# Kernel tuning notes

Hardware: AMD Instinct MI355X
Metric: run time of the kernel (lower is better)

Reference implementation:

```python
import jax, jax.numpy as jnp
import numpy as np

N = 100000   # nodes
E = 1600000  # edges
F_IN = 128
H = 128      # hidden_channels
G = 1000     # graphs in batch
EPS = 1e-5


def setup_inputs() -> dict:
    key = jax.random.key(0)
    ks = jax.random.split(key, 20)
    x = jax.random.normal(ks[0], (N, F_IN), dtype=jnp.float32)
    edge_index = jax.random.randint(ks[1], (2, E), 0, N, dtype=jnp.int64)
    batch = jnp.sort(jax.random.randint(ks[2], (N,), 0, G, dtype=jnp.int64))
    s = 0.05
    inp = {
        "x": x,
        "edge_index": edge_index,
        "batch": batch,
        "W1": jax.random.normal(ks[3], (F_IN, H), dtype=jnp.float32) * s,
        "b1": jnp.zeros((H,), jnp.float32),
        "g1": jnp.ones((H,), jnp.float32),
        "be1": jnp.zeros((H,), jnp.float32),
        "W2": jax.random.normal(ks[4], (H, H), dtype=jnp.float32) * s,
        "b2": jnp.zeros((H,), jnp.float32),
        "g2": jnp.ones((H,), jnp.float32),
        "be2": jnp.zeros((H,), jnp.float32),
        "W3": jax.random.normal(ks[5], (H, H), dtype=jnp.float32) * s,
        "b3": jnp.zeros((H,), jnp.float32),
        "g3": jnp.ones((H,), jnp.float32),
        "be3": jnp.zeros((H,), jnp.float32),
        "Wl": jax.random.normal(ks[6], (H, 1), dtype=jnp.float32) * s,
        "bl": jnp.zeros((1,), jnp.float32),
    }
    return inp


def _gcn_conv(x, W, b, src, dst, dinv):
    # PyG GCNConv: h = x W; out[d] = sum_e dinv[src]*dinv[dst]*h[src]; out += b
    h = x @ W
    coef = (dinv[src] * dinv[dst])[:, None]
    msg = h[src] * coef                       # [E+N, H] gather + scale
    out = jax.ops.segment_sum(msg, dst, num_segments=N)
    return out + b


def _bn_relu(x, g, be):
    # BatchNorm1d training mode: batch stats, biased variance
    m = jnp.mean(x, axis=0)
    v = jnp.var(x, axis=0)
    xn = (x - m) * jax.lax.rsqrt(v + EPS)
    return jax.nn.relu(xn * g + be)


def reference(x, edge_index, batch, W1, b1, g1, be1, W2, b2, g2, be2,
              W3, b3, g3, be3, Wl, bl):
    loop = jnp.arange(N, dtype=edge_index.dtype)
    src = jnp.concatenate([edge_index[0], loop])  # self-loops appended
    dst = jnp.concatenate([edge_index[1], loop])
    deg = jax.ops.segment_sum(jnp.ones_like(dst, dtype=x.dtype), dst,
                              num_segments=N)
    dinv = jax.lax.rsqrt(deg)                     # deg >= 1 (self-loops)

    h = _bn_relu(_gcn_conv(x, W1, b1, src, dst, dinv), g1, be1)
    h = _bn_relu(_gcn_conv(h, W2, b2, src, dst, dinv), g2, be2)
    h = _bn_relu(_gcn_conv(h, W3, b3, src, dst, dinv), g3, be3)

    # global_mean_pool over graph ids
    sums = jax.ops.segment_sum(h, batch, num_segments=G)
    cnt = jax.ops.segment_sum(jnp.ones((N,), h.dtype), batch, num_segments=G)
    pooled = sums / jnp.maximum(cnt, 1.0)[:, None]

    return pooled @ Wl + bl
```

## Files before the change

kernel.cpp:

```cpp
#include <hip/hip_runtime.h>
#include <hip/hip_bf16.h>

#define Nn 100000
#define Ee 1600000
#define Hh 128
#define Gg 1000
#define EPSb 1e-5f

#define SCAN_CHUNK 1024
#define NB_SCAN 98
#define AGG_BLOCKS 2048
#define GEMM_BLOCKS 782

typedef unsigned int uint;
typedef short short8 __attribute__((ext_vector_type(8)));
typedef float floatx4 __attribute__((ext_vector_type(4)));

static __device__ __forceinline__ uint bf16rne(float f) {
    uint u = __float_as_uint(f);
    return (u + 0x7fffu + ((u >> 16) & 1u)) >> 16;
}
static __device__ __forceinline__ float bflo(uint u) { return __uint_as_float(u << 16); }
static __device__ __forceinline__ float bfhi(uint u) { return __uint_as_float(u & 0xffff0000u); }


__global__ void k_init(int* __restrict__ deg, int* __restrict__ cursor,
                       float* __restrict__ colsum) {
    int i = blockIdx.x * blockDim.x + threadIdx.x;
    if (i < Nn) { deg[i] = 1; cursor[i] = 0; }
    if (i < 768) colsum[i] = 0.f;
}

__global__ void k_deg(const int* __restrict__ dst, int* __restrict__ deg) {
    int i = blockIdx.x * blockDim.x + threadIdx.x;
    if (i < Ee) atomicAdd(&deg[dst[i]], 1);
}

__global__ void k_scan1(const int* __restrict__ deg, int* __restrict__ bsum) {
    __shared__ int ls[256];
    int t = threadIdx.x;
    int base = blockIdx.x * SCAN_CHUNK + t * 4;
    int s = 0;
#pragma unroll
    for (int j = 0; j < 4; ++j) { int i = base + j; if (i < Nn) s += deg[i]; }
    ls[t] = s;
    __syncthreads();
    for (int off = 128; off; off >>= 1) {
        if (t < off) ls[t] += ls[t + off];
        __syncthreads();
    }
    if (t == 0) bsum[blockIdx.x] = ls[0];
}

__global__ void k_scan2(int* __restrict__ bsum) {
    __shared__ int ls[128];
    int t = threadIdx.x;
    int v = (t < NB_SCAN) ? bsum[t] : 0;
    ls[t] = v;
    __syncthreads();
    for (int off = 1; off < 128; off <<= 1) {
        int u = (t >= off) ? ls[t - off] : 0;
        __syncthreads();
        ls[t] += u;
        __syncthreads();
    }
    if (t < NB_SCAN) bsum[t] = ls[t] - v;
}

__global__ void k_scan3(const int* __restrict__ deg, const int* __restrict__ bsum,
                        int* __restrict__ offs, float* __restrict__ dinv) {
    __shared__ int ls[256];
    int t = threadIdx.x;
    int base = blockIdx.x * SCAN_CHUNK + t * 4;
    int d[4]; int s = 0;
#pragma unroll
    for (int j = 0; j < 4; ++j) {
        int i = base + j;
        d[j] = (i < Nn) ? deg[i] : 0;
        s += d[j];
    }
    ls[t] = s;
    __syncthreads();
    for (int off = 1; off < 256; off <<= 1) {
        int u = (t >= off) ? ls[t - off] : 0;
        __syncthreads();
        ls[t] += u;
        __syncthreads();
    }
    int run = bsum[blockIdx.x] + ls[t] - s;
#pragma unroll
    for (int j = 0; j < 4; ++j) {
        int i = base + j;
        if (i < Nn) {
            offs[i] = run;
            dinv[i] = rsqrtf((float)d[j]);
        }
        run += d[j];
    }
    if (blockIdx.x == 0 && t == 0) offs[Nn] = Ee + Nn;
}

__global__ void k_fill(const int* __restrict__ src, const int* __restrict__ dst,
                       const int* __restrict__ offs, int* __restrict__ cursor,
                       const float* __restrict__ dinv,
                       int2* __restrict__ adj) {
    int i = blockIdx.x * blockDim.x + threadIdx.x;
    if (i >= Ee + Nn) return;
    int s, d;
    if (i < Ee) { s = src[i]; d = dst[i]; }
    else        { s = d = i - Ee; }
    int pos = offs[d] + atomicAdd(&cursor[d], 1);
    adj[pos] = make_int2(s, __float_as_int(dinv[s] * dinv[d]));
}


__global__ void k_wconv3(const float* __restrict__ W1, const float* __restrict__ W2,
                         const float* __restrict__ W3, uint* __restrict__ Wt) {
    int idx = blockIdx.x * blockDim.x + threadIdx.x;
    if (idx >= 3 * 8192) return;
    const float* W = (idx < 8192) ? W1 : ((idx < 16384) ? W2 : W3);
    int k = idx & 8191;
    int n = k >> 6, ku = k & 63;
    uint lo = bf16rne(W[(size_t)(2 * ku) * 128 + n]);
    uint hi = bf16rne(W[(size_t)(2 * ku + 1) * 128 + n]);
    Wt[(size_t)(idx >> 13) * 8192 + n * 64 + ku] = lo | (hi << 16);
}


__global__ __launch_bounds__(256) void k_gemm(
    const float* __restrict__ inf, const uint* __restrict__ inb,
    const uint* __restrict__ Wtp,
    const float* __restrict__ cs, const float* __restrict__ gg,
    const float* __restrict__ be,
    uint* __restrict__ outb, int mode) {
    __shared__ uint XT[128][64];
    __shared__ uint WT[128][64];
    __shared__ float scsh[256];
    int t = threadIdx.x;
    int rowBase = blockIdx.x * 128;
    int r = t >> 1, half = t & 1;

    if (mode) {
        if (t < 128) {
            float s = cs[t], q = cs[128 + t];
            float m = s * (1.0f / Nn);
            float var = q * (1.0f / Nn) - m * m;
            float istd = rsqrtf(var + EPSb);
            float sc = istd * gg[t];
            scsh[t] = sc;
            scsh[128 + t] = fmaf(-m, sc, be[t]);
        }
        __syncthreads();
    }

    {
        int gr = rowBase + r;
        int grc = gr < Nn ? gr : Nn - 1;
        if (mode == 0) {
            const float* sp = inf + (size_t)grc * 128 + half * 64;
#pragma unroll
            for (int q = 0; q < 8; ++q) {
                float4 v0 = *(const float4*)(sp + q * 8);
                float4 v1 = *(const float4*)(sp + q * 8 + 4);
                uint4 o;
                o.x = bf16rne(v0.x) | (bf16rne(v0.y) << 16);
                o.y = bf16rne(v0.z) | (bf16rne(v0.w) << 16);
                o.z = bf16rne(v1.x) | (bf16rne(v1.y) << 16);
                o.w = bf16rne(v1.z) | (bf16rne(v1.w) << 16);
                int g = half * 8 + q;
                *(uint4*)&XT[r][(g ^ (r & 7)) << 2] = o;
            }
        } else {
            const uint* sp = inb + (size_t)grc * 64 + half * 32;
#pragma unroll
            for (int q = 0; q < 8; ++q) {
                uint4 v = *(const uint4*)(sp + q * 4);
                int fb = half * 64 + q * 8;
                float av[8] = {bflo(v.x), bfhi(v.x), bflo(v.y), bfhi(v.y),
                               bflo(v.z), bfhi(v.z), bflo(v.w), bfhi(v.w)};
                uint o[4];
#pragma unroll
                for (int k2 = 0; k2 < 4; ++k2) {
                    float lo = fmaxf(fmaf(av[2 * k2], scsh[fb + 2 * k2],
                                          scsh[128 + fb + 2 * k2]), 0.f);
                    float hi = fmaxf(fmaf(av[2 * k2 + 1], scsh[fb + 2 * k2 + 1],
                                          scsh[128 + fb + 2 * k2 + 1]), 0.f);
                    o[k2] = bf16rne(lo) | (bf16rne(hi) << 16);
                }
                uint4 ov = make_uint4(o[0], o[1], o[2], o[3]);
                int g = half * 8 + q;
                *(uint4*)&XT[r][(g ^ (r & 7)) << 2] = ov;
            }
        }
    }
    {
        const uint* sp = Wtp + (size_t)r * 64 + half * 32;
#pragma unroll
        for (int q = 0; q < 8; ++q) {
            uint4 v = *(const uint4*)(sp + q * 4);
            int g = half * 8 + q;
            *(uint4*)&WT[r][(g ^ (r & 7)) << 2] = v;
        }
    }
    __syncthreads();

    int l = t & 63, w = t >> 6;
    int nb = (w >> 1) * 64;
    int fb2 = (w & 1) * 64;
    int lr = l & 15, lk = l >> 4;
    floatx4 zero = {0.f, 0.f, 0.f, 0.f};
    floatx4 acc[4][4];
#pragma unroll
    for (int mi = 0; mi < 4; ++mi)
#pragma unroll
        for (int ni = 0; ni < 4; ++ni) acc[mi][ni] = zero;

#pragma unroll
    for (int kc = 0; kc < 4; ++kc) {
        short8 xf[4], wf[4];
        int g = kc * 4 + lk;
#pragma unroll
        for (int mi = 0; mi < 4; ++mi) {
            int rr = nb + mi * 16 + lr;
            xf[mi] = *(const short8*)&XT[rr][(g ^ (rr & 7)) << 2];
        }
#pragma unroll
        for (int ni = 0; ni < 4; ++ni) {
            int rr = fb2 + ni * 16 + lr;
            wf[ni] = *(const short8*)&WT[rr][(g ^ (rr & 7)) << 2];
        }
#pragma unroll
        for (int mi = 0; mi < 4; ++mi)
#pragma unroll
            for (int ni = 0; ni < 4; ++ni)
                acc[mi][ni] = __builtin_amdgcn_mfma_f32_16x16x32_bf16(
                    wf[ni], xf[mi], acc[mi][ni], 0, 0, 0);
    }

#pragma unroll
    for (int mi = 0; mi < 4; ++mi) {
        int node = rowBase + nb + mi * 16 + lr;
        if (node < Nn) {
            uint* op = outb + (size_t)node * 64;
#pragma unroll
            for (int ni = 0; ni < 4; ++ni) {
                int fo = fb2 + ni * 16 + lk * 4;
                uint2 o;
                o.x = bf16rne(acc[mi][ni][0]) | (bf16rne(acc[mi][ni][1]) << 16);
                o.y = bf16rne(acc[mi][ni][2]) | (bf16rne(acc[mi][ni][3]) << 16);
                *(uint2*)(op + (fo >> 1)) = o;
            }
        }
    }
}


__global__ __launch_bounds__(256) void k_agg(
    const uint* __restrict__ h32, const int* __restrict__ offs,
    const int2* __restrict__ adj,
    const float* __restrict__ bias, uint* __restrict__ agg,
    float* __restrict__ colsum) {
    __shared__ float ls[256];
    int tid = threadIdx.x;
    ls[tid] = 0.f;
    __syncthreads();
    int lane = tid & 63;
    int gw = blockIdx.x * 4 + (tid >> 6);
    int nw = AGG_BLOCKS * 4;
    int c0 = lane * 2;
    float b0 = bias[c0], b1 = bias[c0 + 1];
    float ps0 = 0.f, pq0 = 0.f, ps1 = 0.f, pq1 = 0.f;
    for (int d = gw; d < Nn; d += nw) {
        int beg = offs[d], end = offs[d + 1];
        float a0 = 0.f, a1 = 0.f;
        int i = beg;
        for (; i + 8 <= end; i += 8) {
            int2 e[8];
#pragma unroll
            for (int j = 0; j < 8; ++j) e[j] = adj[i + j];
            uint hv[8];
#pragma unroll
            for (int j = 0; j < 8; ++j)
                hv[j] = h32[(size_t)e[j].x * 64 + lane];
#pragma unroll
            for (int j = 0; j < 8; ++j) {
                float w = __int_as_float(e[j].y);
                a0 = fmaf(w, bflo(hv[j]), a0);
                a1 = fmaf(w, bfhi(hv[j]), a1);
            }
        }
        for (; i < end; ++i) {
            int2 e = adj[i];
            uint hv = h32[(size_t)e.x * 64 + lane];
            float w = __int_as_float(e.y);
            a0 = fmaf(w, bflo(hv), a0);
            a1 = fmaf(w, bfhi(hv), a1);
        }
        a0 += b0; a1 += b1;
        agg[(size_t)d * 64 + lane] = bf16rne(a0) | (bf16rne(a1) << 16);
        ps0 += a0; pq0 += a0 * a0;
        ps1 += a1; pq1 += a1 * a1;
    }
    atomicAdd(&ls[c0], ps0);
    atomicAdd(&ls[c0 + 1], ps1);
    atomicAdd(&ls[128 + c0], pq0);
    atomicAdd(&ls[128 + c0 + 1], pq1);
    __syncthreads();
    atomicAdd(&colsum[tid], ls[tid]);
}


__global__ __launch_bounds__(256) void k_pool(
    const uint* __restrict__ agg, const int* __restrict__ batch,
    const float* __restrict__ cs, const float* __restrict__ gg,
    const float* __restrict__ be,
    const float* __restrict__ Wl, const float* __restrict__ bl,
    float* __restrict__ out) {
    __shared__ float scsh[256];
    int tid = threadIdx.x;
    if (tid < 128) {
        float s = cs[tid], q = cs[128 + tid];
        float m = s * (1.0f / Nn);
        float var = q * (1.0f / Nn) - m * m;
        float istd = rsqrtf(var + EPSb);
        float sc = istd * gg[tid];
        scsh[tid] = sc;
        scsh[128 + tid] = fmaf(-m, sc, be[tid]);
    }
    __syncthreads();
    int lane = tid & 63;
    int g = (blockIdx.x * blockDim.x + tid) >> 6;
    if (g >= Gg) return;
    int lo = 0, hi = Nn;
    while (lo < hi) { int mid = (lo + hi) >> 1; if (batch[mid] < g) lo = mid + 1; else hi = mid; }
    int beg = lo;
    hi = Nn;
    while (lo < hi) { int mid = (lo + hi) >> 1; if (batch[mid] < g + 1) lo = mid + 1; else hi = mid; }
    int end = lo;
    int c0 = lane * 2;
    float sc0 = scsh[c0], sh0 = scsh[128 + c0];
    float sc1 = scsh[c0 + 1], sh1 = scsh[128 + c0 + 1];
    float s0 = 0.f, s1 = 0.f;
    for (int n = beg; n < end; ++n) {
        uint v = agg[(size_t)n * 64 + lane];
        s0 += fmaxf(fmaf(bflo(v), sc0, sh0), 0.f);
        s1 += fmaxf(fmaf(bfhi(v), sc1, sh1), 0.f);
    }
    float inv = 1.0f / fmaxf((float)(end - beg), 1.0f);
    float part = (s0 * inv) * Wl[c0] + (s1 * inv) * Wl[c0 + 1];
#pragma unroll
    for (int off = 32; off; off >>= 1) part += __shfl_down(part, off);
    if (lane == 0) out[g] = part + bl[0];
}


extern "C" void kernel_launch(void* const* d_in, const int* in_sizes, int n_in,
                              void* d_out, int out_size, void* d_ws, size_t ws_size,
                              hipStream_t stream) {
    const float* x   = (const float*)d_in[0];
    const int*   ei  = (const int*)d_in[1];
    const int*   src = ei;
    const int*   dst = ei + Ee;
    const int*   bat = (const int*)d_in[2];
    const float* W1 = (const float*)d_in[3];
    const float* b1 = (const float*)d_in[4];
    const float* g1 = (const float*)d_in[5];
    const float* be1 = (const float*)d_in[6];
    const float* W2 = (const float*)d_in[7];
    const float* b2 = (const float*)d_in[8];
    const float* g2 = (const float*)d_in[9];
    const float* be2 = (const float*)d_in[10];
    const float* W3 = (const float*)d_in[11];
    const float* b3 = (const float*)d_in[12];
    const float* g3 = (const float*)d_in[13];
    const float* be3 = (const float*)d_in[14];
    const float* Wl = (const float*)d_in[15];
    const float* bl = (const float*)d_in[16];
    float* out = (float*)d_out;

    char* w = (char*)d_ws;
    auto alloc = [&](size_t bytes) {
        void* p = (void*)w;
        w += (bytes + 255) & ~(size_t)255;
        return p;
    };
    int*   deg    = (int*)alloc((size_t)Nn * 4);
    int*   cursor = (int*)alloc((size_t)Nn * 4);
    int*   offs   = (int*)alloc((size_t)(Nn + 1) * 4);
    int*   bsum   = (int*)alloc(256 * 4);
    float* dinv   = (float*)alloc((size_t)Nn * 4);
    float* colsum = (float*)alloc(768 * 4);
    uint*  Wt     = (uint*)alloc((size_t)3 * 8192 * 4);
    int2*  adj    = (int2*)alloc((size_t)(Ee + Nn) * 8);
    uint*  tmp    = (uint*)alloc((size_t)Nn * 64 * 4);
    uint*  agg    = (uint*)alloc((size_t)Nn * 64 * 4);

    float* csA = colsum;
    float* csB = colsum + 256;
    float* csC = colsum + 512;

    k_init<<<(Nn + 255) / 256, 256, 0, stream>>>(deg, cursor, colsum);
    k_deg<<<(Ee + 255) / 256, 256, 0, stream>>>(dst, deg);
    k_scan1<<<NB_SCAN, 256, 0, stream>>>(deg, bsum);
    k_scan2<<<1, 128, 0, stream>>>(bsum);
    k_scan3<<<NB_SCAN, 256, 0, stream>>>(deg, bsum, offs, dinv);
    k_fill<<<(Ee + Nn + 255) / 256, 256, 0, stream>>>(src, dst, offs, cursor, dinv, adj);
    k_wconv3<<<96, 256, 0, stream>>>(W1, W2, W3, Wt);
    k_gemm<<<GEMM_BLOCKS, 256, 0, stream>>>(x, (const uint*)0, Wt,
                                            (const float*)0, (const float*)0,
                                            (const float*)0, tmp, 0);
    k_agg<<<AGG_BLOCKS, 256, 0, stream>>>(tmp, offs, adj, b1, agg, csA);
    k_gemm<<<GEMM_BLOCKS, 256, 0, stream>>>((const float*)0, agg, Wt + 8192,
                                            csA, g1, be1, tmp, 1);
    k_agg<<<AGG_BLOCKS, 256, 0, stream>>>(tmp, offs, adj, b2, agg, csB);
    k_gemm<<<GEMM_BLOCKS, 256, 0, stream>>>((const float*)0, agg, Wt + 16384,
                                            csB, g2, be2, tmp, 1);
    k_agg<<<AGG_BLOCKS, 256, 0, stream>>>(tmp, offs, adj, b3, agg, csC);
    k_pool<<<(Gg * 64 + 255) / 256, 256, 0, stream>>>(agg, bat, csC, g3, be3,
                                                      Wl, bl, out);
}
```

Before: 598.5 us.

## Gather 16-byte row slices across four edge groups per wave in aggregation

Each wave now splits into four 16-lane groups that each take a different edge. Every lane loads a uint4 (8 bf16 features) per edge instead of one uint, and the groups' partial sums are combined with cross-lane shuffles before lane group 0 writes the row and updates the BN statistics. The aim is wider, fewer gather instructions and more edges in flight per wave in the memory-bound aggregation. The cost is extra shuffle reductions and predicated tail handling that does masked loads. Only a quarter of the lanes do the final store and stats work.

```diff
diff --git a/kernel.cpp b/kernel.cpp
--- a/kernel.cpp
+++ b/kernel.cpp
@@ -10,9 +10,11 @@
 #define SCAN_CHUNK 1024
 #define NB_SCAN 98
 #define AGG_BLOCKS 2048
+#define NWAVES (AGG_BLOCKS * 4)
 #define GEMM_BLOCKS 782
 
 typedef unsigned int uint;
+typedef unsigned long long u64;
 typedef short short8 __attribute__((ext_vector_type(8)));
 typedef float floatx4 __attribute__((ext_vector_type(4)));
 
@@ -265,46 +267,93 @@
     ls[tid] = 0.f;
     __syncthreads();
     int lane = tid & 63;
-    int gw = blockIdx.x * 4 + (tid >> 6);
-    int nw = AGG_BLOCKS * 4;
-    int c0 = lane * 2;
-    float b0 = bias[c0], b1 = bias[c0 + 1];
-    float ps0 = 0.f, pq0 = 0.f, ps1 = 0.f, pq1 = 0.f;
-    for (int d = gw; d < Nn; d += nw) {
+    int g = lane >> 4;
+    int c = lane & 15;
+    int wv = blockIdx.x * 4 + (tid >> 6);
+    const uint4* h4 = (const uint4*)h32;
+    const u64* adj8 = (const u64*)adj;
+    int f0 = c * 8;
+    float bb[8];
+#pragma unroll
+    for (int j = 0; j < 8; ++j) bb[j] = bias[f0 + j];
+    float ps[8], pq[8];
+#pragma unroll
+    for (int j = 0; j < 8; ++j) { ps[j] = 0.f; pq[j] = 0.f; }
+
+    for (int d = wv; d < Nn; d += NWAVES) {
         int beg = offs[d], end = offs[d + 1];
-        float a0 = 0.f, a1 = 0.f;
+        float acc[8];
+#pragma unroll
+        for (int j = 0; j < 8; ++j) acc[j] = 0.f;
         int i = beg;
         for (; i + 8 <= end; i += 8) {
-            int2 e[8];
-#pragma unroll
-            for (int j = 0; j < 8; ++j) e[j] = adj[i + j];
-            uint hv[8];
-#pragma unroll
-            for (int j = 0; j < 8; ++j)
-                hv[j] = h32[(size_t)e[j].x * 64 + lane];
+            u64 eA = adj8[i + g];
+            u64 eB = adj8[i + 4 + g];
+            uint4 hA = h4[(size_t)(uint)eA * 16 + c];
+            uint4 hB = h4[(size_t)(uint)eB * 16 + c];
+            float wA = __uint_as_float((uint)(eA >> 32));
+            float wB = __uint_as_float((uint)(eB >> 32));
+            acc[0] = fmaf(wA, bflo(hA.x), acc[0]);
+            acc[1] = fmaf(wA, bfhi(hA.x), acc[1]);
+            acc[2] = fmaf(wA, bflo(hA.y), acc[2]);
+            acc[3] = fmaf(wA, bfhi(hA.y), acc[3]);
+            acc[4] = fmaf(wA, bflo(hA.z), acc[4]);
+            acc[5] = fmaf(wA, bfhi(hA.z), acc[5]);
+            acc[6] = fmaf(wA, bflo(hA.w), acc[6]);
+            acc[7] = fmaf(wA, bfhi(hA.w), acc[7]);
+            acc[0] = fmaf(wB, bflo(hB.x), acc[0]);
+            acc[1] = fmaf(wB, bfhi(hB.x), acc[1]);
+            acc[2] = fmaf(wB, bflo(hB.y), acc[2]);
+            acc[3] = fmaf(wB, bfhi(hB.y), acc[3]);
+            acc[4] = fmaf(wB, bflo(hB.z), acc[4]);
+            acc[5] = fmaf(wB, bfhi(hB.z), acc[5]);
+            acc[6] = fmaf(wB, bflo(hB.w), acc[6]);
+            acc[7] = fmaf(wB, bfhi(hB.w), acc[7]);
+        }
+        for (; i < end; i += 4) {
+            int idx = i + g;
+            int ok = idx < end;
+            u64 e = adj8[ok ? idx : (end - 1)];
+            uint4 hv = h4[(size_t)(uint)e * 16 + c];
+            float w = ok ? __uint_as_float((uint)(e >> 32)) : 0.f;
+            acc[0] = fmaf(w, bflo(hv.x), acc[0]);
+            acc[1] = fmaf(w, bfhi(hv.x), acc[1]);
+            acc[2] = fmaf(w, bflo(hv.y), acc[2]);
+            acc[3] = fmaf(w, bfhi(hv.y), acc[3]);
+            acc[4] = fmaf(w, bflo(hv.z), acc[4]);
+            acc[5] = fmaf(w, bfhi(hv.z), acc[5]);
+            acc[6] = fmaf(w, bflo(hv.w), acc[6]);
+            acc[7] = fmaf(w, bfhi(hv.w), acc[7]);
+        }
+#pragma unroll
+        for (int j = 0; j < 8; ++j) {
+            acc[j] += __shfl_xor(acc[j], 16);
+            acc[j] += __shfl_xor(acc[j], 32);
+        }
+        if (g == 0) {
+            float a[8];
+#pragma unroll
+            for (int j = 0; j < 8; ++j) a[j] = acc[j] + bb[j];
+            uint4 o;
+            o.x = bf16rne(a[0]) | (bf16rne(a[1]) << 16);
+            o.y = bf16rne(a[2]) | (bf16rne(a[3]) << 16);
+            o.z = bf16rne(a[4]) | (bf16rne(a[5]) << 16);
+            o.w = bf16rne(a[6]) | (bf16rne(a[7]) << 16);
+            *(uint4*)(agg + (size_t)d * 64 + c * 4) = o;
 #pragma unroll
             for (int j = 0; j < 8; ++j) {
-                float w = __int_as_float(e[j].y);
-                a0 = fmaf(w, bflo(hv[j]), a0);
-                a1 = fmaf(w, bfhi(hv[j]), a1);
+                ps[j] += a[j];
+                pq[j] += a[j] * a[j];
             }
         }
-        for (; i < end; ++i) {
-            int2 e = adj[i];
-            uint hv = h32[(size_t)e.x * 64 + lane];
-            float w = __int_as_float(e.y);
-            a0 = fmaf(w, bflo(hv), a0);
-            a1 = fmaf(w, bfhi(hv), a1);
-        }
-        a0 += b0; a1 += b1;
-        agg[(size_t)d * 64 + lane] = bf16rne(a0) | (bf16rne(a1) << 16);
-        ps0 += a0; pq0 += a0 * a0;
-        ps1 += a1; pq1 += a1 * a1;
-    }
-    atomicAdd(&ls[c0], ps0);
-    atomicAdd(&ls[c0 + 1], ps1);
-    atomicAdd(&ls[128 + c0], pq0);
-    atomicAdd(&ls[128 + c0 + 1], pq1);
+    }
+    if (g == 0) {
+#pragma unroll
+        for (int j = 0; j < 8; ++j) {
+            atomicAdd(&ls[f0 + j], ps[j]);
+            atomicAdd(&ls[128 + f0 + j], pq[j]);
+        }
+    }
     __syncthreads();
     atomicAdd(&colsum[tid], ls[tid]);
 }
```

After: 647.5 us. 1.08x slower.

## Process two row tiles per GEMM block with prefetch; merge scan passes and memset init

Applied to the files above, without the earlier changes.

The GEMM kernel now handles two 128-row tiles per block, with half as many blocks. It loads the second tile's inputs into registers while the first tile's MFMAs run, so the global-load latency is hidden and the weight tile is loaded once for both. The init kernel is replaced by a single hipMemsetAsync over deg, cursor and colsum, and the self-loop +1 is folded into the scan reads. The separate block-sum scan kernel is merged into scan3, which saves launches. In exchange, registers rise from holding the prefetched tile (launch bounds set to 2 blocks per SM), and every scan3 block redundantly rescans the block sums.

```diff
diff --git a/kernel.cpp b/kernel.cpp
--- a/kernel.cpp
+++ b/kernel.cpp
@@ -10,7 +10,8 @@
 #define SCAN_CHUNK 1024
 #define NB_SCAN 98
 #define AGG_BLOCKS 2048
-#define GEMM_BLOCKS 782
+#define NWAVES (AGG_BLOCKS * 4)
+#define GEMM_BLOCKS 391
 
 typedef unsigned int uint;
 typedef short short8 __attribute__((ext_vector_type(8)));
@@ -23,13 +24,6 @@
 static __device__ __forceinline__ float bflo(uint u) { return __uint_as_float(u << 16); }
 static __device__ __forceinline__ float bfhi(uint u) { return __uint_as_float(u & 0xffff0000u); }
 
-
-__global__ void k_init(int* __restrict__ deg, int* __restrict__ cursor,
-                       float* __restrict__ colsum) {
-    int i = blockIdx.x * blockDim.x + threadIdx.x;
-    if (i < Nn) { deg[i] = 1; cursor[i] = 0; }
-    if (i < 768) colsum[i] = 0.f;
-}
 
 __global__ void k_deg(const int* __restrict__ dst, int* __restrict__ deg) {
     int i = blockIdx.x * blockDim.x + threadIdx.x;
@@ -42,7 +36,7 @@
     int base = blockIdx.x * SCAN_CHUNK + t * 4;
     int s = 0;
 #pragma unroll
-    for (int j = 0; j < 4; ++j) { int i = base + j; if (i < Nn) s += deg[i]; }
+    for (int j = 0; j < 4; ++j) { int i = base + j; if (i < Nn) s += deg[i] + 1; }
     ls[t] = s;
     __syncthreads();
     for (int off = 128; off; off >>= 1) {
@@ -52,42 +46,36 @@
     if (t == 0) bsum[blockIdx.x] = ls[0];
 }
 
-__global__ void k_scan2(int* __restrict__ bsum) {
-    __shared__ int ls[128];
-    int t = threadIdx.x;
-    int v = (t < NB_SCAN) ? bsum[t] : 0;
-    ls[t] = v;
-    __syncthreads();
-    for (int off = 1; off < 128; off <<= 1) {
-        int u = (t >= off) ? ls[t - off] : 0;
-        __syncthreads();
-        ls[t] += u;
-        __syncthreads();
-    }
-    if (t < NB_SCAN) bsum[t] = ls[t] - v;
-}
-
 __global__ void k_scan3(const int* __restrict__ deg, const int* __restrict__ bsum,
                         int* __restrict__ offs, float* __restrict__ dinv) {
     __shared__ int ls[256];
+    __shared__ int bs[128];
     int t = threadIdx.x;
+    if (t < 128) bs[t] = (t < NB_SCAN) ? bsum[t] : 0;
     int base = blockIdx.x * SCAN_CHUNK + t * 4;
     int d[4]; int s = 0;
 #pragma unroll
     for (int j = 0; j < 4; ++j) {
         int i = base + j;
-        d[j] = (i < Nn) ? deg[i] : 0;
+        d[j] = (i < Nn) ? deg[i] + 1 : 0;
         s += d[j];
     }
     ls[t] = s;
     __syncthreads();
+    for (int off = 1; off < 128; off <<= 1) {
+        int u = (t >= off && t < 128) ? bs[t - off] : 0;
+        __syncthreads();
+        if (t < 128) bs[t] += u;
+        __syncthreads();
+    }
     for (int off = 1; off < 256; off <<= 1) {
         int u = (t >= off) ? ls[t - off] : 0;
         __syncthreads();
         ls[t] += u;
         __syncthreads();
     }
-    int run = bsum[blockIdx.x] + ls[t] - s;
+    int blockBase = (blockIdx.x == 0) ? 0 : bs[blockIdx.x - 1];
+    int run = blockBase + ls[t] - s;
 #pragma unroll
     for (int j = 0; j < 4; ++j) {
         int i = base + j;
@@ -127,7 +115,7 @@
 }
 
 
-__global__ __launch_bounds__(256) void k_gemm(
+__global__ __launch_bounds__(256, 2) void k_gemm(
     const float* __restrict__ inf, const uint* __restrict__ inb,
     const uint* __restrict__ Wtp,
     const float* __restrict__ cs, const float* __restrict__ gg,
@@ -137,61 +125,16 @@
     __shared__ uint WT[128][64];
     __shared__ float scsh[256];
     int t = threadIdx.x;
-    int rowBase = blockIdx.x * 128;
     int r = t >> 1, half = t & 1;
 
-    if (mode) {
-        if (t < 128) {
-            float s = cs[t], q = cs[128 + t];
-            float m = s * (1.0f / Nn);
-            float var = q * (1.0f / Nn) - m * m;
-            float istd = rsqrtf(var + EPSb);
-            float sc = istd * gg[t];
-            scsh[t] = sc;
-            scsh[128 + t] = fmaf(-m, sc, be[t]);
-        }
-        __syncthreads();
-    }
-
-    {
-        int gr = rowBase + r;
-        int grc = gr < Nn ? gr : Nn - 1;
-        if (mode == 0) {
-            const float* sp = inf + (size_t)grc * 128 + half * 64;
-#pragma unroll
-            for (int q = 0; q < 8; ++q) {
-                float4 v0 = *(const float4*)(sp + q * 8);
-                float4 v1 = *(const float4*)(sp + q * 8 + 4);
-                uint4 o;
-                o.x = bf16rne(v0.x) | (bf16rne(v0.y) << 16);
-                o.y = bf16rne(v0.z) | (bf16rne(v0.w) << 16);
-                o.z = bf16rne(v1.x) | (bf16rne(v1.y) << 16);
-                o.w = bf16rne(v1.z) | (bf16rne(v1.w) << 16);
-                int g = half * 8 + q;
-                *(uint4*)&XT[r][(g ^ (r & 7)) << 2] = o;
-            }
-        } else {
-            const uint* sp = inb + (size_t)grc * 64 + half * 32;
-#pragma unroll
-            for (int q = 0; q < 8; ++q) {
-                uint4 v = *(const uint4*)(sp + q * 4);
-                int fb = half * 64 + q * 8;
-                float av[8] = {bflo(v.x), bfhi(v.x), bflo(v.y), bfhi(v.y),
-                               bflo(v.z), bfhi(v.z), bflo(v.w), bfhi(v.w)};
-                uint o[4];
-#pragma unroll
-                for (int k2 = 0; k2 < 4; ++k2) {
-                    float lo = fmaxf(fmaf(av[2 * k2], scsh[fb + 2 * k2],
-                                          scsh[128 + fb + 2 * k2]), 0.f);
-                    float hi = fmaxf(fmaf(av[2 * k2 + 1], scsh[fb + 2 * k2 + 1],
-                                          scsh[128 + fb + 2 * k2 + 1]), 0.f);
-                    o[k2] = bf16rne(lo) | (bf16rne(hi) << 16);
-                }
-                uint4 ov = make_uint4(o[0], o[1], o[2], o[3]);
-                int g = half * 8 + q;
-                *(uint4*)&XT[r][(g ^ (r & 7)) << 2] = ov;
-            }
-        }
+    if (mode && t < 128) {
+        float s = cs[t], q = cs[128 + t];
+        float m = s * (1.0f / Nn);
+        float var = q * (1.0f / Nn) - m * m;
+        float istd = rsqrtf(var + EPSb);
+        float sc = istd * gg[t];
+        scsh[t] = sc;
+        scsh[128 + t] = fmaf(-m, sc, be[t]);
     }
     {
         const uint* sp = Wtp + (size_t)r * 64 + half * 32;
@@ -201,6 +144,57 @@
             int g = half * 8 + q;
             *(uint4*)&WT[r][(g ^ (r & 7)) << 2] = v;
         }
+    }
+
+    float4 xf[16];
+    uint4  xb[8];
+
+    int rb0 = blockIdx.x * 128;
+    {
+        int grc = rb0 + r;
+        if (grc >= Nn) grc = Nn - 1;
+        if (mode == 0) {
+            const float* sp = inf + (size_t)grc * 128 + half * 64;
+#pragma unroll
+            for (int q = 0; q < 8; ++q) {
+                xf[2 * q]     = *(const float4*)(sp + q * 8);
+                xf[2 * q + 1] = *(const float4*)(sp + q * 8 + 4);
+            }
+        } else {
+            const uint* sp = inb + (size_t)grc * 64 + half * 32;
+#pragma unroll
+            for (int q = 0; q < 8; ++q) xb[q] = *(const uint4*)(sp + q * 4);
+        }
+    }
+    __syncthreads();
+
+#pragma unroll
+    for (int q = 0; q < 8; ++q) {
+        uint4 o;
+        if (mode == 0) {
+            float4 v0 = xf[2 * q], v1 = xf[2 * q + 1];
+            o.x = bf16rne(v0.x) | (bf16rne(v0.y) << 16);
+            o.y = bf16rne(v0.z) | (bf16rne(v0.w) << 16);
+            o.z = bf16rne(v1.x) | (bf16rne(v1.y) << 16);
+            o.w = bf16rne(v1.z) | (bf16rne(v1.w) << 16);
+        } else {
+            uint4 v = xb[q];
+            int fb = half * 64 + q * 8;
+            float av[8] = {bflo(v.x), bfhi(v.x), bflo(v.y), bfhi(v.y),
+                           bflo(v.z), bfhi(v.z), bflo(v.w), bfhi(v.w)};
+            uint oo[4];
+#pragma unroll
+            for (int k2 = 0; k2 < 4; ++k2) {
+                float lo = fmaxf(fmaf(av[2 * k2], scsh[fb + 2 * k2],
+                                      scsh[128 + fb + 2 * k2]), 0.f);
+                float hi = fmaxf(fmaf(av[2 * k2 + 1], scsh[fb + 2 * k2 + 1],
+                                      scsh[128 + fb + 2 * k2 + 1]), 0.f);
+                oo[k2] = bf16rne(lo) | (bf16rne(hi) << 16);
+            }
+            o = make_uint4(oo[0], oo[1], oo[2], oo[3]);
+        }
+        int g = half * 8 + q;
+        *(uint4*)&XT[r][(g ^ (r & 7)) << 2] = o;
     }
     __syncthreads();
 
@@ -209,46 +203,140 @@
     int fb2 = (w & 1) * 64;
     int lr = l & 15, lk = l >> 4;
     floatx4 zero = {0.f, 0.f, 0.f, 0.f};
-    floatx4 acc[4][4];
-#pragma unroll
-    for (int mi = 0; mi < 4; ++mi)
-#pragma unroll
-        for (int ni = 0; ni < 4; ++ni) acc[mi][ni] = zero;
-
-#pragma unroll
-    for (int kc = 0; kc < 4; ++kc) {
-        short8 xf[4], wf[4];
-        int g = kc * 4 + lk;
+
+    int rb1 = (blockIdx.x + GEMM_BLOCKS) * 128;
+    {
+        int grc = rb1 + r;
+        if (grc >= Nn) grc = Nn - 1;
+        if (mode == 0) {
+            const float* sp = inf + (size_t)grc * 128 + half * 64;
+#pragma unroll
+            for (int q = 0; q < 8; ++q) {
+                xf[2 * q]     = *(const float4*)(sp + q * 8);
+                xf[2 * q + 1] = *(const float4*)(sp + q * 8 + 4);
+            }
+        } else {
+            const uint* sp = inb + (size_t)grc * 64 + half * 32;
+#pragma unroll
+            for (int q = 0; q < 8; ++q) xb[q] = *(const uint4*)(sp + q * 4);
+        }
+    }
+
+    {
+        floatx4 acc[4][4];
+#pragma unroll
+        for (int mi = 0; mi < 4; ++mi)
+#pragma unroll
+            for (int ni = 0; ni < 4; ++ni) acc[mi][ni] = zero;
+#pragma unroll
+        for (int kc = 0; kc < 4; ++kc) {
+            short8 xfr[4], wfr[4];
+            int g = kc * 4 + lk;
+#pragma unroll
+            for (int mi = 0; mi < 4; ++mi) {
+                int rr = nb + mi * 16 + lr;
+                xfr[mi] = *(const short8*)&XT[rr][(g ^ (rr & 7)) << 2];
+            }
+#pragma unroll
+            for (int ni = 0; ni < 4; ++ni) {
+                int rr = fb2 + ni * 16 + lr;
+                wfr[ni] = *(const short8*)&WT[rr][(g ^ (rr & 7)) << 2];
+            }
+#pragma unroll
+            for (int mi = 0; mi < 4; ++mi)
+#pragma unroll
+                for (int ni = 0; ni < 4; ++ni)
+                    acc[mi][ni] = __builtin_amdgcn_mfma_f32_16x16x32_bf16(
+                        wfr[ni], xfr[mi], acc[mi][ni], 0, 0, 0);
+        }
 #pragma unroll
         for (int mi = 0; mi < 4; ++mi) {
-            int rr = nb + mi * 16 + lr;
-            xf[mi] = *(const short8*)&XT[rr][(g ^ (rr & 7)) << 2];
-        }
-#pragma unroll
-        for (int ni = 0; ni < 4; ++ni) {
-            int rr = fb2 + ni * 16 + lr;
-            wf[ni] = *(const short8*)&WT[rr][(g ^ (rr & 7)) << 2];
-        }
+            int node = rb0 + nb + mi * 16 + lr;
+            if (node < Nn) {
+                uint* op = outb + (size_t)node * 64;
+#pragma unroll
+                for (int ni = 0; ni < 4; ++ni) {
+                    int fo = fb2 + ni * 16 + lk * 4;
+                    uint2 o;
+                    o.x = bf16rne(acc[mi][ni][0]) | (bf16rne(acc[mi][ni][1]) << 16);
+                    o.y = bf16rne(acc[mi][ni][2]) | (bf16rne(acc[mi][ni][3]) << 16);
+                    *(uint2*)(op + (fo >> 1)) = o;
+                }
+            }
+        }
+    }
+    __syncthreads();
+
+#pragma unroll
+    for (int q = 0; q < 8; ++q) {
+        uint4 o;
+        if (mode == 0) {
+            float4 v0 = xf[2 * q], v1 = xf[2 * q + 1];
+            o.x = bf16rne(v0.x) | (bf16rne(v0.y) << 16);
+            o.y = bf16rne(v0.z) | (bf16rne(v0.w) << 16);
+            o.z = bf16rne(v1.x) | (bf16rne(v1.y) << 16);
+            o.w = bf16rne(v1.z) | (bf16rne(v1.w) << 16);
+        } else {
+            uint4 v = xb[q];
+            int fb = half * 64 + q * 8;
+            float av[8] = {bflo(v.x), bfhi(v.x), bflo(v.y), bfhi(v.y),
+                           bflo(v.z), bfhi(v.z), bflo(v.w), bfhi(v.w)};
+            uint oo[4];
+#pragma unroll
+            for (int k2 = 0; k2 < 4; ++k2) {
+                float lo = fmaxf(fmaf(av[2 * k2], scsh[fb + 2 * k2],
+                                      scsh[128 + fb + 2 * k2]), 0.f);
+                float hi = fmaxf(fmaf(av[2 * k2 + 1], scsh[fb + 2 * k2 + 1],
+                                      scsh[128 + fb + 2 * k2 + 1]), 0.f);
+                oo[k2] = bf16rne(lo) | (bf16rne(hi) << 16);
+            }
+            o = make_uint4(oo[0], oo[1], oo[2], oo[3]);
+        }
+        int g = half * 8 + q;
+        *(uint4*)&XT[r][(g ^ (r & 7)) << 2] = o;
+    }
+    __syncthreads();
+
+    {
+        floatx4 acc[4][4];
 #pragma unroll
         for (int mi = 0; mi < 4; ++mi)
 #pragma unroll
-            for (int ni = 0; ni < 4; ++ni)
-                acc[mi][ni] = __builtin_amdgcn_mfma_f32_16x16x32_bf16(
-                    wf[ni], xf[mi], acc[mi][ni], 0, 0, 0);
-    }
-
-#pragma unroll
-    for (int mi = 0; mi < 4; ++mi) {
-        int node = rowBase + nb + mi * 16 + lr;
-        if (node < Nn) {
-            uint* op = outb + (size_t)node * 64;
+            for (int ni = 0; ni < 4; ++ni) acc[mi][ni] = zero;
+#pragma unroll
+        for (int kc = 0; kc < 4; ++kc) {
+            short8 xfr[4], wfr[4];
+            int g = kc * 4 + lk;
+#pragma unroll
+            for (int mi = 0; mi < 4; ++mi) {
+                int rr = nb + mi * 16 + lr;
+                xfr[mi] = *(const short8*)&XT[rr][(g ^ (rr & 7)) << 2];
+            }
 #pragma unroll
             for (int ni = 0; ni < 4; ++ni) {
-                int fo = fb2 + ni * 16 + lk * 4;
-                uint2 o;
-                o.x = bf16rne(acc[mi][ni][0]) | (bf16rne(acc[mi][ni][1]) << 16);
-                o.y = bf16rne(acc[mi][ni][2]) | (bf16rne(acc[mi][ni][3]) << 16);
-                *(uint2*)(op + (fo >> 1)) = o;
+                int rr = fb2 + ni * 16 + lr;
+                wfr[ni] = *(const short8*)&WT[rr][(g ^ (rr & 7)) << 2];
+            }
+#pragma unroll
+            for (int mi = 0; mi < 4; ++mi)
+#pragma unroll
+                for (int ni = 0; ni < 4; ++ni)
+                    acc[mi][ni] = __builtin_amdgcn_mfma_f32_16x16x32_bf16(
+                        wfr[ni], xfr[mi], acc[mi][ni], 0, 0, 0);
+        }
+#pragma unroll
+        for (int mi = 0; mi < 4; ++mi) {
+            int node = rb1 + nb + mi * 16 + lr;
+            if (node < Nn) {
+                uint* op = outb + (size_t)node * 64;
+#pragma unroll
+                for (int ni = 0; ni < 4; ++ni) {
+                    int fo = fb2 + ni * 16 + lk * 4;
+                    uint2 o;
+                    o.x = bf16rne(acc[mi][ni][0]) | (bf16rne(acc[mi][ni][1]) << 16);
+                    o.y = bf16rne(acc[mi][ni][2]) | (bf16rne(acc[mi][ni][3]) << 16);
+                    *(uint2*)(op + (fo >> 1)) = o;
+                }
             }
         }
     }
@@ -266,7 +354,7 @@
     __syncthreads();
     int lane = tid & 63;
     int gw = blockIdx.x * 4 + (tid >> 6);
-    int nw = AGG_BLOCKS * 4;
+    int nw = NWAVES;
     int c0 = lane * 2;
     float b0 = bias[c0], b1 = bias[c0 + 1];
     float ps0 = 0.f, pq0 = 0.f, ps1 = 0.f, pq1 = 0.f;
@@ -386,10 +474,11 @@
     };
     int*   deg    = (int*)alloc((size_t)Nn * 4);
     int*   cursor = (int*)alloc((size_t)Nn * 4);
+    float* colsum = (float*)alloc(768 * 4);
+    size_t zspan  = (size_t)((char*)(colsum + 768) - (char*)deg);
     int*   offs   = (int*)alloc((size_t)(Nn + 1) * 4);
     int*   bsum   = (int*)alloc(256 * 4);
     float* dinv   = (float*)alloc((size_t)Nn * 4);
-    float* colsum = (float*)alloc(768 * 4);
     uint*  Wt     = (uint*)alloc((size_t)3 * 8192 * 4);
     int2*  adj    = (int2*)alloc((size_t)(Ee + Nn) * 8);
     uint*  tmp    = (uint*)alloc((size_t)Nn * 64 * 4);
@@ -399,10 +488,9 @@
     float* csB = colsum + 256;
     float* csC = colsum + 512;
 
-    k_init<<<(Nn + 255) / 256, 256, 0, stream>>>(deg, cursor, colsum);
+    hipMemsetAsync(deg, 0, zspan, stream);
     k_deg<<<(Ee + 255) / 256, 256, 0, stream>>>(dst, deg);
     k_scan1<<<NB_SCAN, 256, 0, stream>>>(deg, bsum);
-    k_scan2<<<1, 128, 0, stream>>>(bsum);
     k_scan3<<<NB_SCAN, 256, 0, stream>>>(deg, bsum, offs, dinv);
     k_fill<<<(Ee + Nn + 255) / 256, 256, 0, stream>>>(src, dst, offs, cursor, dinv, adj);
     k_wconv3<<<96, 256, 0, stream>>>(W1, W2, W3, Wt);
```

Result: no change. 595.4 us (-0.5%).

## Factor GCN normalization into GEMM epilogue and shrink adjacency to source indices

Applied to the files above, without the earlier changes.

The GCN edge weight dinv[src]*dinv[dst] is split. The source factor is applied in the GEMM epilogue before the bf16 store, and the destination factor is applied once per node after summation in the aggregation. This lets the CSR adjacency hold only 4-byte source indices instead of 8-byte (index, weight) pairs, halving adjacency traffic in each of the three aggregation passes and in the fill. It also replaces the init kernel with a memset, folds the self-loop +1 into the scan reads, and merges the second scan stage into the third. Rounding changes slightly because the pre-scaled features are stored in bf16.

```diff
diff --git a/kernel.cpp b/kernel.cpp
--- a/kernel.cpp
+++ b/kernel.cpp
@@ -10,6 +10,7 @@
 #define SCAN_CHUNK 1024
 #define NB_SCAN 98
 #define AGG_BLOCKS 2048
+#define NWAVES (AGG_BLOCKS * 4)
 #define GEMM_BLOCKS 782
 
 typedef unsigned int uint;
@@ -23,13 +24,6 @@
 static __device__ __forceinline__ float bflo(uint u) { return __uint_as_float(u << 16); }
 static __device__ __forceinline__ float bfhi(uint u) { return __uint_as_float(u & 0xffff0000u); }
 
-
-__global__ void k_init(int* __restrict__ deg, int* __restrict__ cursor,
-                       float* __restrict__ colsum) {
-    int i = blockIdx.x * blockDim.x + threadIdx.x;
-    if (i < Nn) { deg[i] = 1; cursor[i] = 0; }
-    if (i < 768) colsum[i] = 0.f;
-}
 
 __global__ void k_deg(const int* __restrict__ dst, int* __restrict__ deg) {
     int i = blockIdx.x * blockDim.x + threadIdx.x;
@@ -42,7 +36,7 @@
     int base = blockIdx.x * SCAN_CHUNK + t * 4;
     int s = 0;
 #pragma unroll
-    for (int j = 0; j < 4; ++j) { int i = base + j; if (i < Nn) s += deg[i]; }
+    for (int j = 0; j < 4; ++j) { int i = base + j; if (i < Nn) s += deg[i] + 1; }
     ls[t] = s;
     __syncthreads();
     for (int off = 128; off; off >>= 1) {
@@ -50,44 +44,38 @@
         __syncthreads();
     }
     if (t == 0) bsum[blockIdx.x] = ls[0];
-}
-
-__global__ void k_scan2(int* __restrict__ bsum) {
-    __shared__ int ls[128];
-    int t = threadIdx.x;
-    int v = (t < NB_SCAN) ? bsum[t] : 0;
-    ls[t] = v;
-    __syncthreads();
-    for (int off = 1; off < 128; off <<= 1) {
-        int u = (t >= off) ? ls[t - off] : 0;
-        __syncthreads();
-        ls[t] += u;
-        __syncthreads();
-    }
-    if (t < NB_SCAN) bsum[t] = ls[t] - v;
 }
 
 __global__ void k_scan3(const int* __restrict__ deg, const int* __restrict__ bsum,
                         int* __restrict__ offs, float* __restrict__ dinv) {
     __shared__ int ls[256];
+    __shared__ int bs[128];
     int t = threadIdx.x;
+    if (t < 128) bs[t] = (t < NB_SCAN) ? bsum[t] : 0;
     int base = blockIdx.x * SCAN_CHUNK + t * 4;
     int d[4]; int s = 0;
 #pragma unroll
     for (int j = 0; j < 4; ++j) {
         int i = base + j;
-        d[j] = (i < Nn) ? deg[i] : 0;
+        d[j] = (i < Nn) ? deg[i] + 1 : 0;
         s += d[j];
     }
     ls[t] = s;
     __syncthreads();
+    for (int off = 1; off < 128; off <<= 1) {
+        int u = (t >= off && t < 128) ? bs[t - off] : 0;
+        __syncthreads();
+        if (t < 128) bs[t] += u;
+        __syncthreads();
+    }
     for (int off = 1; off < 256; off <<= 1) {
         int u = (t >= off) ? ls[t - off] : 0;
         __syncthreads();
         ls[t] += u;
         __syncthreads();
     }
-    int run = bsum[blockIdx.x] + ls[t] - s;
+    int blockBase = (blockIdx.x == 0) ? 0 : bs[blockIdx.x - 1];
+    int run = blockBase + ls[t] - s;
 #pragma unroll
     for (int j = 0; j < 4; ++j) {
         int i = base + j;
@@ -102,15 +90,14 @@
 
 __global__ void k_fill(const int* __restrict__ src, const int* __restrict__ dst,
                        const int* __restrict__ offs, int* __restrict__ cursor,
-                       const float* __restrict__ dinv,
-                       int2* __restrict__ adj) {
+                       int* __restrict__ adj) {
     int i = blockIdx.x * blockDim.x + threadIdx.x;
     if (i >= Ee + Nn) return;
     int s, d;
     if (i < Ee) { s = src[i]; d = dst[i]; }
     else        { s = d = i - Ee; }
     int pos = offs[d] + atomicAdd(&cursor[d], 1);
-    adj[pos] = make_int2(s, __float_as_int(dinv[s] * dinv[d]));
+    adj[pos] = s;
 }
 
 
@@ -129,7 +116,7 @@
 
 __global__ __launch_bounds__(256) void k_gemm(
     const float* __restrict__ inf, const uint* __restrict__ inb,
-    const uint* __restrict__ Wtp,
+    const uint* __restrict__ Wtp, const float* __restrict__ dinv,
     const float* __restrict__ cs, const float* __restrict__ gg,
     const float* __restrict__ be,
     uint* __restrict__ outb, int mode) {
@@ -241,13 +228,14 @@
     for (int mi = 0; mi < 4; ++mi) {
         int node = rowBase + nb + mi * 16 + lr;
         if (node < Nn) {
+            float dv = dinv[node];
             uint* op = outb + (size_t)node * 64;
 #pragma unroll
             for (int ni = 0; ni < 4; ++ni) {
                 int fo = fb2 + ni * 16 + lk * 4;
                 uint2 o;
-                o.x = bf16rne(acc[mi][ni][0]) | (bf16rne(acc[mi][ni][1]) << 16);
-                o.y = bf16rne(acc[mi][ni][2]) | (bf16rne(acc[mi][ni][3]) << 16);
+                o.x = bf16rne(acc[mi][ni][0] * dv) | (bf16rne(acc[mi][ni][1] * dv) << 16);
+                o.y = bf16rne(acc[mi][ni][2] * dv) | (bf16rne(acc[mi][ni][3] * dv) << 16);
                 *(uint2*)(op + (fo >> 1)) = o;
             }
         }
@@ -257,7 +245,7 @@
 
 __global__ __launch_bounds__(256) void k_agg(
     const uint* __restrict__ h32, const int* __restrict__ offs,
-    const int2* __restrict__ adj,
+    const int* __restrict__ adj, const float* __restrict__ dinv,
     const float* __restrict__ bias, uint* __restrict__ agg,
     float* __restrict__ colsum) {
     __shared__ float ls[256];
@@ -266,37 +254,36 @@
     __syncthreads();
     int lane = tid & 63;
     int gw = blockIdx.x * 4 + (tid >> 6);
-    int nw = AGG_BLOCKS * 4;
+    int nw = NWAVES;
     int c0 = lane * 2;
     float b0 = bias[c0], b1 = bias[c0 + 1];
     float ps0 = 0.f, pq0 = 0.f, ps1 = 0.f, pq1 = 0.f;
     for (int d = gw; d < Nn; d += nw) {
         int beg = offs[d], end = offs[d + 1];
+        float dvd = dinv[d];
         float a0 = 0.f, a1 = 0.f;
         int i = beg;
         for (; i + 8 <= end; i += 8) {
-            int2 e[8];
+            int e[8];
 #pragma unroll
             for (int j = 0; j < 8; ++j) e[j] = adj[i + j];
             uint hv[8];
 #pragma unroll
             for (int j = 0; j < 8; ++j)
-                hv[j] = h32[(size_t)e[j].x * 64 + lane];
+                hv[j] = h32[(size_t)e[j] * 64 + lane];
 #pragma unroll
             for (int j = 0; j < 8; ++j) {
-                float w = __int_as_float(e[j].y);
-                a0 = fmaf(w, bflo(hv[j]), a0);
-                a1 = fmaf(w, bfhi(hv[j]), a1);
+                a0 += bflo(hv[j]);
+                a1 += bfhi(hv[j]);
             }
         }
         for (; i < end; ++i) {
-            int2 e = adj[i];
-            uint hv = h32[(size_t)e.x * 64 + lane];
-            float w = __int_as_float(e.y);
-            a0 = fmaf(w, bflo(hv), a0);
-            a1 = fmaf(w, bfhi(hv), a1);
-        }
-        a0 += b0; a1 += b1;
+            uint hv = h32[(size_t)adj[i] * 64 + lane];
+            a0 += bflo(hv);
+            a1 += bfhi(hv);
+        }
+        a0 = fmaf(a0, dvd, b0);
+        a1 = fmaf(a1, dvd, b1);
         agg[(size_t)d * 64 + lane] = bf16rne(a0) | (bf16rne(a1) << 16);
         ps0 += a0; pq0 += a0 * a0;
         ps1 += a1; pq1 += a1 * a1;
@@ -386,12 +373,13 @@
     };
     int*   deg    = (int*)alloc((size_t)Nn * 4);
     int*   cursor = (int*)alloc((size_t)Nn * 4);
+    float* colsum = (float*)alloc(768 * 4);
+    size_t zspan  = (size_t)((char*)(colsum + 768) - (char*)deg);
     int*   offs   = (int*)alloc((size_t)(Nn + 1) * 4);
     int*   bsum   = (int*)alloc(256 * 4);
     float* dinv   = (float*)alloc((size_t)Nn * 4);
-    float* colsum = (float*)alloc(768 * 4);
     uint*  Wt     = (uint*)alloc((size_t)3 * 8192 * 4);
-    int2*  adj    = (int2*)alloc((size_t)(Ee + Nn) * 8);
+    int*   adj    = (int*)alloc((size_t)(Ee + Nn) * 4);
     uint*  tmp    = (uint*)alloc((size_t)Nn * 64 * 4);
     uint*  agg    = (uint*)alloc((size_t)Nn * 64 * 4);
 
@@ -399,23 +387,22 @@
     float* csB = colsum + 256;
     float* csC = colsum + 512;
 
-    k_init<<<(Nn + 255) / 256, 256, 0, stream>>>(deg, cursor, colsum);
+    hipMemsetAsync(deg, 0, zspan, stream);
     k_deg<<<(Ee + 255) / 256, 256, 0, stream>>>(dst, deg);
     k_scan1<<<NB_SCAN, 256, 0, stream>>>(deg, bsum);
-    k_scan2<<<1, 128, 0, stream>>>(bsum);
     k_scan3<<<NB_SCAN, 256, 0, stream>>>(deg, bsum, offs, dinv);
-    k_fill<<<(Ee + Nn + 255) / 256, 256, 0, stream>>>(src, dst, offs, cursor, dinv, adj);
+    k_fill<<<(Ee + Nn + 255) / 256, 256, 0, stream>>>(src, dst, offs, cursor, adj);
     k_wconv3<<<96, 256, 0, stream>>>(W1, W2, W3, Wt);
-    k_gemm<<<GEMM_BLOCKS, 256, 0, stream>>>(x, (const uint*)0, Wt,
+    k_gemm<<<GEMM_BLOCKS, 256, 0, stream>>>(x, (const uint*)0, Wt, dinv,
                                             (const float*)0, (const float*)0,
                                             (const float*)0, tmp, 0);
-    k_agg<<<AGG_BLOCKS, 256, 0, stream>>>(tmp, offs, adj, b1, agg, csA);
-    k_gemm<<<GEMM_BLOCKS, 256, 0, stream>>>((const float*)0, agg, Wt + 8192,
+    k_agg<<<AGG_BLOCKS, 256, 0, stream>>>(tmp, offs, adj, dinv, b1, agg, csA);
+    k_gemm<<<GEMM_BLOCKS, 256, 0, stream>>>((const float*)0, agg, Wt + 8192, dinv,
                                             csA, g1, be1, tmp, 1);
-    k_agg<<<AGG_BLOCKS, 256, 0, stream>>>(tmp, offs, adj, b2, agg, csB);
-    k_gemm<<<GEMM_BLOCKS, 256, 0, stream>>>((const float*)0, agg, Wt + 16384,
+    k_agg<<<AGG_BLOCKS, 256, 0, stream>>>(tmp, offs, adj, dinv, b2, agg, csB);
+    k_gemm<<<GEMM_BLOCKS, 256, 0, stream>>>((const float*)0, agg, Wt + 16384, dinv,
                                             csB, g2, be2, tmp, 1);
-    k_agg<<<AGG_BLOCKS, 256, 0, stream>>>(tmp, offs, adj, b3, agg, csC);
+    k_agg<<<AGG_BLOCKS, 256, 0, stream>>>(tmp, offs, adj, dinv, b3, agg, csC);
     k_pool<<<(Gg * 64 + 255) / 256, 256, 0, stream>>>(agg, bat, csC, g3, be3,
                                                       Wl, bl, out);
 }
```

After: 629.8 us. 1.05x slower.
